# Optimization experiments

Measured on AMD Instinct MI355X. Metric: run time of the kernel, lower is better.

Reference implementation:

```python
import jax, jax.numpy as jnp
import numpy as np

N_NODES = 50000
N_EDGES = 800000
D_IN = 128
D_OUT = 128

def setup_inputs() -> dict:
    key = jax.random.key(0)
    k1, k2, k3, k4, k5, k6 = jax.random.split(key, 6)
    adj_row = jax.random.randint(k1, (N_EDGES,), 0, N_NODES, dtype=jnp.int32)
    adj_col = jax.random.randint(k2, (N_EDGES,), 0, N_NODES, dtype=jnp.int32)
    adj_vals = jax.random.uniform(k3, (N_EDGES,), dtype=jnp.float32)
    features = jax.random.normal(k4, (N_NODES, D_IN), dtype=jnp.float32)
    W = jax.random.normal(k5, (D_OUT, D_IN), dtype=jnp.float32) * (1.0 / np.sqrt(D_IN))
    b = jax.random.normal(k6, (D_OUT,), dtype=jnp.float32) * 0.01
    return {"adj_row": adj_row, "adj_col": adj_col, "adj_vals": adj_vals,
            "features": features, "W": W, "b": b}

def reference(adj_row, adj_col, adj_vals, features, W, b):
    # SpMM: f[i] = sum_{e: row[e]=i} vals[e] * features[col[e]]
    msgs = adj_vals[:, None] * features[adj_col]          # [E, D_IN]
    f = jax.ops.segment_sum(msgs, adj_row, num_segments=N_NODES)  # [N, D_IN]
    # dense linear: f @ W.T + b  (nn.Linear convention)
    out = jnp.einsum('nd,od->no', f, W) + b               # [N, D_OUT]
    return out
```

## Files before the change

kernel.cpp:

```cpp
#include <hip/hip_runtime.h>
#include <hip/hip_fp16.h>

#define N_NODES 50000
#define N_EDGES 800000
#define D 128
#define PAD 56
#define NPART 8
#define NCHUNK 391

typedef __attribute__((ext_vector_type(8))) short bf16x8;
typedef __attribute__((ext_vector_type(4))) float f32x4;

#define WS_H_OFF      0
#define WS_ECSR_OFF   12800000
#define WS_COUNTS_OFF 24000000
#define WS_REC_OFF    24200000

__device__ __forceinline__ unsigned int f2bf(float f) {
    unsigned int u = __float_as_uint(f);
    unsigned int r = u + 0x7FFFu + ((u >> 16) & 1u);
    return r >> 16;
}
__device__ __forceinline__ float bf_lo(unsigned int u) {
    return __uint_as_float(u << 16);
}
__device__ __forceinline__ float bf_hi(unsigned int u) {
    return __uint_as_float(u & 0xFFFF0000u);
}
__device__ __forceinline__ int part_of(unsigned int row) {
    return (int)((row * 687195ull) >> 32);
}

__global__ void pack_rec_kernel(const int* __restrict__ row,
                                const int* __restrict__ col,
                                const float* __restrict__ vals,
                                int2* __restrict__ rec) {
    int i = blockIdx.x * blockDim.x + threadIdx.x;
    int e = i * 4;
    if (e >= N_EDGES) return;
    int4   rr = *reinterpret_cast<const int4*>(row + e);
    int4   cc = *reinterpret_cast<const int4*>(col + e);
    float4 vv = *reinterpret_cast<const float4*>(vals + e);
    rec[e + 0] = make_int2((rr.x << 16) | cc.x, __float_as_int(vv.x));
    rec[e + 1] = make_int2((rr.y << 16) | cc.y, __float_as_int(vv.y));
    rec[e + 2] = make_int2((rr.z << 16) | cc.z, __float_as_int(vv.z));
    rec[e + 3] = make_int2((rr.w << 16) | cc.w, __float_as_int(vv.w));
}

__global__ __launch_bounds__(256) void csr_build_kernel(
        const int2* __restrict__ rec, int* __restrict__ counts,
        unsigned int* __restrict__ ecsr) {
    const int p     = blockIdx.x & 7;
    const int chunk = blockIdx.x >> 3;
    const int t     = threadIdx.x;

    #pragma unroll
    for (int i = 0; i < 8; ++i) {
        int e = chunk * 2048 + i * 256 + t;
        if (e < N_EDGES) {
            int2 r = rec[e];
            unsigned int row = ((unsigned int)r.x) >> 16;
            if (part_of(row) == p) {
                int k = atomicAdd(&counts[row], 1);
                unsigned int c16 = (unsigned int)r.x & 0xFFFFu;
                unsigned int h = __half_as_ushort(__float2half_rn(__int_as_float(r.y)));
                if (k < PAD) ecsr[row * PAD + k] = c16 | (h << 16);
            }
        }
    }
}

__global__ __launch_bounds__(256) void gemm_mfma_kernel(
        const float* __restrict__ X, const float* __restrict__ W,
        unsigned int* __restrict__ H16) {
    __shared__ unsigned int Wlds[128 * 64];
    const int t = threadIdx.x;

    char* lw = (char*)Wlds;
    #pragma unroll
    for (int i = 0; i < 16; ++i) {
        int idx4 = t + i * 256;
        float4 w4 = reinterpret_cast<const float4*>(W)[idx4];
        int row = idx4 >> 5;
        int kq  = idx4 & 31;
        int byte = (row * 256 + kq * 8) ^ ((row & 7) << 4);
        uint2 p;
        p.x = f2bf(w4.x) | (f2bf(w4.y) << 16);
        p.y = f2bf(w4.z) | (f2bf(w4.w) << 16);
        *reinterpret_cast<uint2*>(lw + byte) = p;
    }
    __syncthreads();

    const int w    = t >> 6;
    const int lane = t & 63;
    const int lrow = lane & 15;
    const int lk   = lane >> 4;

    const int xrow   = blockIdx.x * 64 + w * 16 + lrow;
    const int xrow_c = (xrow < N_NODES) ? xrow : (N_NODES - 1);

    const float4* Xr = reinterpret_cast<const float4*>(X + (size_t)xrow_c * D);
    bf16x8 xb[4];
    #pragma unroll
    for (int ks = 0; ks < 4; ++ks) {
        float4 a = Xr[ks * 8 + lk * 2];
        float4 bq = Xr[ks * 8 + lk * 2 + 1];
        bf16x8 v;
        v[0] = (short)f2bf(a.x);  v[1] = (short)f2bf(a.y);
        v[2] = (short)f2bf(a.z);  v[3] = (short)f2bf(a.w);
        v[4] = (short)f2bf(bq.x); v[5] = (short)f2bf(bq.y);
        v[6] = (short)f2bf(bq.z); v[7] = (short)f2bf(bq.w);
        xb[ks] = v;
    }

    const char* lr = (const char*)Wlds;
    #pragma unroll
    for (int n0 = 0; n0 < 8; ++n0) {
        f32x4 acc = {0.f, 0.f, 0.f, 0.f};
        #pragma unroll
        for (int ks = 0; ks < 4; ++ks) {
            int wrow = n0 * 16 + lrow;
            int byte = (wrow * 256 + ks * 64 + lk * 16) ^ ((wrow & 7) << 4);
            bf16x8 af = *reinterpret_cast<const bf16x8*>(lr + byte);
            acc = __builtin_amdgcn_mfma_f32_16x16x32_bf16(af, xb[ks], acc, 0, 0, 0);
        }
        if (xrow < N_NODES) {
            uint2 p;
            p.x = f2bf(acc[0]) | (f2bf(acc[1]) << 16);
            p.y = f2bf(acc[2]) | (f2bf(acc[3]) << 16);
            *reinterpret_cast<uint2*>(H16 + (size_t)xrow * 64 + n0 * 8 + (lk << 1)) = p;
        }
    }
}

__global__ __launch_bounds__(256) void aggregate_kernel(
        const int* __restrict__ counts, const unsigned int* __restrict__ ecsr,
        const unsigned int* __restrict__ H16,
        const float* __restrict__ b, float* __restrict__ out) {
    int gtid = blockIdx.x * blockDim.x + threadIdx.x;
    int row  = gtid >> 6;
    int lane = threadIdx.x & 63;
    if (row >= N_NODES) return;

    const int eg = lane >> 4;
    const int c  = lane & 15;

    int deg = counts[row];
    if (deg > PAD) deg = PAD;
    const unsigned int* seg = ecsr + row * PAD;

    float a[8];
    #pragma unroll
    for (int k = 0; k < 8; ++k) a[k] = 0.f;

    #define EDGE_BODY(IDX)                                                        \
        {                                                                         \
            unsigned int rc = seg[(IDX)];                                         \
            int   cx = rc & 0xFFFFu;                                              \
            float v  = __half2float(__ushort_as_half((unsigned short)(rc >> 16)));\
            uint4 h = *reinterpret_cast<const uint4*>(H16 + (size_t)cx * 64 + c * 4);\
            a[0] += v * bf_lo(h.x); a[1] += v * bf_hi(h.x);                       \
            a[2] += v * bf_lo(h.y); a[3] += v * bf_hi(h.y);                       \
            a[4] += v * bf_lo(h.z); a[5] += v * bf_hi(h.z);                       \
            a[6] += v * bf_lo(h.w); a[7] += v * bf_hi(h.w);                       \
        }

    int i = eg;
    for (; i + 4 < deg; i += 8) {
        EDGE_BODY(i);
        EDGE_BODY(i + 4);
    }
    if (i < deg) EDGE_BODY(i);
    #undef EDGE_BODY

    #pragma unroll
    for (int k = 0; k < 8; ++k) {
        a[k] += __shfl_xor(a[k], 16, 64);
        a[k] += __shfl_xor(a[k], 32, 64);
    }

    if (eg == 0) {
        float4 b0 = *reinterpret_cast<const float4*>(b + c * 8);
        float4 b1 = *reinterpret_cast<const float4*>(b + c * 8 + 4);
        float4 o0 = {a[0] + b0.x, a[1] + b0.y, a[2] + b0.z, a[3] + b0.w};
        float4 o1 = {a[4] + b1.x, a[5] + b1.y, a[6] + b1.z, a[7] + b1.w};
        float* dst = out + (size_t)row * D + c * 8;
        *reinterpret_cast<float4*>(dst)     = o0;
        *reinterpret_cast<float4*>(dst + 4) = o1;
    }
}

extern "C" void kernel_launch(void* const* d_in, const int* in_sizes, int n_in,
                              void* d_out, int out_size, void* d_ws, size_t ws_size,
                              hipStream_t stream) {
    const int*   adj_row  = (const int*)d_in[0];
    const int*   adj_col  = (const int*)d_in[1];
    const float* adj_vals = (const float*)d_in[2];
    const float* features = (const float*)d_in[3];
    const float* W        = (const float*)d_in[4];
    const float* b        = (const float*)d_in[5];
    float*       out      = (float*)d_out;

    char* ws = (char*)d_ws;
    unsigned int* H16    = (unsigned int*)(ws + WS_H_OFF);
    unsigned int* ecsr   = (unsigned int*)(ws + WS_ECSR_OFF);
    int*          counts = (int*)(ws + WS_COUNTS_OFF);
    int2*         rec    = (int2*)(ws + WS_REC_OFF);

    hipMemsetAsync(counts, 0, N_NODES * sizeof(int), stream);
    pack_rec_kernel<<<(N_EDGES / 4 + 255) / 256, 256, 0, stream>>>(
        adj_row, adj_col, adj_vals, rec);
    csr_build_kernel<<<NCHUNK * NPART, 256, 0, stream>>>(rec, counts, ecsr);
    gemm_mfma_kernel<<<(N_NODES + 63) / 64, 256, 0, stream>>>(features, W, H16);
    {
        int blocks = (N_NODES * 64 + 255) / 256;
        aggregate_kernel<<<blocks, 256, 0, stream>>>(counts, ecsr, H16, b, out);
    }
}
```

Measured before the change: 97.37 us.

## Bucket edges by row partition before CSR build instead of re-scanning all edges

Replaces the pack kernel plus the 8x partitioned CSR scan, in which every block read all edge records for its chunk and kept only one partition, with a bucketing pass. That pass writes each edge into a per-partition queue using block-local LDS counters and one global atomic per partition. The CSR build then reads only its partition's queue, which removes the eightfold redundant reads of the record array. The memset is folded into the pack kernel and the queue-counter reset into the GEMM, which now runs first. The queues have a fixed capacity, so a badly skewed partition would drop edges.

```diff
diff --git a/kernel.cpp b/kernel.cpp
--- a/kernel.cpp
+++ b/kernel.cpp
@@ -6,7 +6,9 @@
 #define D 128
 #define PAD 56
 #define NPART 8
-#define NCHUNK 391
+#define QCAP 131072
+#define CSR_BPP 98
+#define PACK_BLOCKS 782
 
 typedef __attribute__((ext_vector_type(8))) short bf16x8;
 typedef __attribute__((ext_vector_type(4))) float f32x4;
@@ -14,7 +16,8 @@
 #define WS_H_OFF      0
 #define WS_ECSR_OFF   12800000
 #define WS_COUNTS_OFF 24000000
-#define WS_REC_OFF    24200000
+#define WS_QCNT_OFF   24200000
+#define WS_QUEUE_OFF  24200064
 
 __device__ __forceinline__ unsigned int f2bf(float f) {
     unsigned int u = __float_as_uint(f);
@@ -31,50 +34,76 @@
     return (int)((row * 687195ull) >> 32);
 }
 
-__global__ void pack_rec_kernel(const int* __restrict__ row,
-                                const int* __restrict__ col,
-                                const float* __restrict__ vals,
-                                int2* __restrict__ rec) {
-    int i = blockIdx.x * blockDim.x + threadIdx.x;
-    int e = i * 4;
-    if (e >= N_EDGES) return;
-    int4   rr = *reinterpret_cast<const int4*>(row + e);
-    int4   cc = *reinterpret_cast<const int4*>(col + e);
-    float4 vv = *reinterpret_cast<const float4*>(vals + e);
-    rec[e + 0] = make_int2((rr.x << 16) | cc.x, __float_as_int(vv.x));
-    rec[e + 1] = make_int2((rr.y << 16) | cc.y, __float_as_int(vv.y));
-    rec[e + 2] = make_int2((rr.z << 16) | cc.z, __float_as_int(vv.z));
-    rec[e + 3] = make_int2((rr.w << 16) | cc.w, __float_as_int(vv.w));
-}
-
-__global__ __launch_bounds__(256) void csr_build_kernel(
-        const int2* __restrict__ rec, int* __restrict__ counts,
-        unsigned int* __restrict__ ecsr) {
-    const int p     = blockIdx.x & 7;
-    const int chunk = blockIdx.x >> 3;
-    const int t     = threadIdx.x;
-
-    #pragma unroll
-    for (int i = 0; i < 8; ++i) {
-        int e = chunk * 2048 + i * 256 + t;
-        if (e < N_EDGES) {
-            int2 r = rec[e];
-            unsigned int row = ((unsigned int)r.x) >> 16;
-            if (part_of(row) == p) {
-                int k = atomicAdd(&counts[row], 1);
-                unsigned int c16 = (unsigned int)r.x & 0xFFFFu;
-                unsigned int h = __half_as_ushort(__float2half_rn(__int_as_float(r.y)));
-                if (k < PAD) ecsr[row * PAD + k] = c16 | (h << 16);
-            }
-        }
+__global__ __launch_bounds__(256) void pack_bucket_kernel(
+        const int* __restrict__ row, const int* __restrict__ col,
+        const float* __restrict__ vals,
+        int* __restrict__ counts, int* __restrict__ qcnt,
+        int2* __restrict__ queue) {
+    __shared__ int lcnt[NPART];
+    __shared__ int lbase[NPART];
+    const int t = threadIdx.x;
+
+    int gid = blockIdx.x * 256 + t;
+    if (gid < N_NODES) counts[gid] = 0;
+    if (t < NPART) lcnt[t] = 0;
+    __syncthreads();
+
+    const int e0 = blockIdx.x * 1024 + t * 4;
+    int  r[4], c[4], pp[4], rk[4];
+    float v[4];
+    bool valid = (e0 < N_EDGES);
+    if (valid) {
+        int4   rr = *reinterpret_cast<const int4*>(row + e0);
+        int4   cc = *reinterpret_cast<const int4*>(col + e0);
+        float4 vv = *reinterpret_cast<const float4*>(vals + e0);
+        r[0] = rr.x; r[1] = rr.y; r[2] = rr.z; r[3] = rr.w;
+        c[0] = cc.x; c[1] = cc.y; c[2] = cc.z; c[3] = cc.w;
+        v[0] = vv.x; v[1] = vv.y; v[2] = vv.z; v[3] = vv.w;
+        #pragma unroll
+        for (int j = 0; j < 4; ++j) {
+            pp[j] = part_of((unsigned int)r[j]);
+            rk[j] = atomicAdd(&lcnt[pp[j]], 1);
+        }
+    }
+    __syncthreads();
+    if (t < NPART) lbase[t] = atomicAdd(&qcnt[t], lcnt[t]);
+    __syncthreads();
+    if (valid) {
+        #pragma unroll
+        for (int j = 0; j < 4; ++j) {
+            int pos = lbase[pp[j]] + rk[j];
+            if (pos < QCAP)
+                queue[pp[j] * QCAP + pos] =
+                    make_int2((r[j] << 16) | c[j], __float_as_int(v[j]));
+        }
+    }
+}
+
+__global__ __launch_bounds__(256) void csr_build2_kernel(
+        const int2* __restrict__ queue, const int* __restrict__ qcnt,
+        int* __restrict__ counts, unsigned int* __restrict__ ecsr) {
+    const int p  = blockIdx.x & 7;
+    const int bi = blockIdx.x >> 3;
+    int n = qcnt[p];
+    if (n > QCAP) n = QCAP;
+    const int2* q = queue + p * QCAP;
+
+    for (int i = bi * 256 + threadIdx.x; i < n; i += CSR_BPP * 256) {
+        int2 rec = q[i];
+        unsigned int row = ((unsigned int)rec.x) >> 16;
+        int k = atomicAdd(&counts[row], 1);
+        unsigned int c16 = (unsigned int)rec.x & 0xFFFFu;
+        unsigned int h = __half_as_ushort(__float2half_rn(__int_as_float(rec.y)));
+        if (k < PAD) ecsr[row * PAD + k] = c16 | (h << 16);
     }
 }
 
 __global__ __launch_bounds__(256) void gemm_mfma_kernel(
         const float* __restrict__ X, const float* __restrict__ W,
-        unsigned int* __restrict__ H16) {
+        unsigned int* __restrict__ H16, int* __restrict__ qcnt) {
     __shared__ unsigned int Wlds[128 * 64];
     const int t = threadIdx.x;
+    if (blockIdx.x == 0 && t < NPART) qcnt[t] = 0;
 
     char* lw = (char*)Wlds;
     #pragma unroll
@@ -103,14 +132,14 @@
     bf16x8 xb[4];
     #pragma unroll
     for (int ks = 0; ks < 4; ++ks) {
-        float4 a = Xr[ks * 8 + lk * 2];
+        float4 a  = Xr[ks * 8 + lk * 2];
         float4 bq = Xr[ks * 8 + lk * 2 + 1];
-        bf16x8 v;
-        v[0] = (short)f2bf(a.x);  v[1] = (short)f2bf(a.y);
-        v[2] = (short)f2bf(a.z);  v[3] = (short)f2bf(a.w);
-        v[4] = (short)f2bf(bq.x); v[5] = (short)f2bf(bq.y);
-        v[6] = (short)f2bf(bq.z); v[7] = (short)f2bf(bq.w);
-        xb[ks] = v;
+        bf16x8 vv;
+        vv[0] = (short)f2bf(a.x);  vv[1] = (short)f2bf(a.y);
+        vv[2] = (short)f2bf(a.z);  vv[3] = (short)f2bf(a.w);
+        vv[4] = (short)f2bf(bq.x); vv[5] = (short)f2bf(bq.y);
+        vv[6] = (short)f2bf(bq.z); vv[7] = (short)f2bf(bq.w);
+        xb[ks] = vv;
     }
 
     const char* lr = (const char*)Wlds;
@@ -205,13 +234,13 @@
     unsigned int* H16    = (unsigned int*)(ws + WS_H_OFF);
     unsigned int* ecsr   = (unsigned int*)(ws + WS_ECSR_OFF);
     int*          counts = (int*)(ws + WS_COUNTS_OFF);
-    int2*         rec    = (int2*)(ws + WS_REC_OFF);
-
-    hipMemsetAsync(counts, 0, N_NODES * sizeof(int), stream);
-    pack_rec_kernel<<<(N_EDGES / 4 + 255) / 256, 256, 0, stream>>>(
-        adj_row, adj_col, adj_vals, rec);
-    csr_build_kernel<<<NCHUNK * NPART, 256, 0, stream>>>(rec, counts, ecsr);
-    gemm_mfma_kernel<<<(N_NODES + 63) / 64, 256, 0, stream>>>(features, W, H16);
+    int*          qcnt   = (int*) (ws + WS_QCNT_OFF);
+    int2*         queue  = (int2*)(ws + WS_QUEUE_OFF);
+
+    gemm_mfma_kernel<<<(N_NODES + 63) / 64, 256, 0, stream>>>(features, W, H16, qcnt);
+    pack_bucket_kernel<<<PACK_BLOCKS, 256, 0, stream>>>(
+        adj_row, adj_col, adj_vals, counts, qcnt, queue);
+    csr_build2_kernel<<<CSR_BPP * NPART, 256, 0, stream>>>(queue, qcnt, counts, ecsr);
     {
         int blocks = (N_NODES * 64 + 255) / 256;
         aggregate_kernel<<<blocks, 256, 0, stream>>>(counts, ecsr, H16, b, out);
```

New measurement: 100.2 us. +2.9%, slower.
